# Optimization experiments

Measured on AMD Instinct MI355X. Metric: run time of the kernel, lower is better.

The kernel has to match this reference:

```python
import jax, jax.numpy as jnp
import numpy as np

HEADS = 8
DIM_HEAD = 64
SCALE = DIM_HEAD ** -0.5


def setup_inputs() -> dict:
    key = jax.random.key(0)
    k1, k2, k3 = jax.random.split(key, 3)
    b, p, n, dim = 2, 16, 512, 512
    inner = HEADS * DIM_HEAD  # 512
    x = jax.random.normal(k1, (b, p, n, dim), dtype=jnp.float32)
    W_qkv = jax.random.normal(k2, (dim, 3 * inner), dtype=jnp.float32) * (dim ** -0.5)
    W_out = jax.random.normal(k3, (inner, dim), dtype=jnp.float32) * (inner ** -0.5)
    b_out = jnp.zeros((dim,), dtype=jnp.float32)
    return {"x": x, "W_qkv": W_qkv, "W_out": W_out, "b_out": b_out}


def reference(x, W_qkv, W_out, b_out):
    b, p, n, dim = x.shape
    # QKV projection (no bias), split into q, k, v
    qkv = jnp.einsum('bpnd,de->bpne', x, W_qkv)
    q, k, v = jnp.split(qkv, 3, axis=-1)
    # (b, p, n, h*d) -> (b, p, h, n, d)
    def to_heads(t):
        return t.reshape(b, p, n, HEADS, DIM_HEAD).transpose(0, 1, 3, 2, 4)
    q, k, v = to_heads(q), to_heads(k), to_heads(v)
    # attention scores: (b, p, h, n, n)
    dots = jnp.einsum('bphnd,bphmd->bphnm', q, k) * SCALE
    attn = jax.nn.softmax(dots, axis=-1)
    out = jnp.einsum('bphnm,bphmd->bphnd', attn, v)
    # (b, p, h, n, d) -> (b, p, n, h*d)
    out = out.transpose(0, 1, 3, 2, 4).reshape(b, p, n, HEADS * DIM_HEAD)
    # output projection (dropout rate = 0.0 -> identity)
    return jnp.einsum('bpne,ed->bpnd', out, W_out) + b_out
```

## Files before the change

### kernel.cpp

```cpp
#include <hip/hip_runtime.h>
#include <hip/hip_bf16.h>

typedef short bf16x8 __attribute__((ext_vector_type(8)));
typedef short bf16x4 __attribute__((ext_vector_type(4)));
typedef float f32x4  __attribute__((ext_vector_type(4)));

__device__ __forceinline__ unsigned short f2bf(float f) {
    union { float fv; unsigned int u; } v; v.fv = f;
    unsigned int r = v.u + 0x7FFFu + ((v.u >> 16) & 1u);
    return (unsigned short)(r >> 16);
}

__device__ __forceinline__ short f2bf_n(float f) {
    union { __hip_bfloat16 h; short s; } u;
    u.h = __float2bfloat16(f);
    return u.s;
}

__device__ __forceinline__ void gload16(const short* g, short* l) {
    __builtin_amdgcn_global_load_lds(
        (const __attribute__((address_space(1))) void*)g,
        (__attribute__((address_space(3))) void*)l, 16, 0, 0);
}

__global__ __launch_bounds__(256) void cvt_x(
    const float* __restrict__ x, short* __restrict__ xb)
{
    size_t i = ((size_t)blockIdx.x * 256 + threadIdx.x) * 8;
    f32x4 a = *(const f32x4*)(x + i);
    f32x4 b = *(const f32x4*)(x + i + 4);
    bf16x8 s;
    #pragma unroll
    for (int e = 0; e < 4; ++e) { s[e] = (short)f2bf(a[e]); s[4 + e] = (short)f2bf(b[e]); }
    *(bf16x8*)(xb + i) = s;
}

__global__ __launch_bounds__(256) void tr_w2(
    const float* __restrict__ Wqkv, const float* __restrict__ Wout,
    short* __restrict__ Wqkvt, short* __restrict__ Woutt)
{
    __shared__ float tile[32][33];
    const int b = blockIdx.x;
    const float* src; short* dst; int N, bb;
    if (b < 768) { src = Wqkv; dst = Wqkvt; N = 1536; bb = b; }
    else         { src = Wout; dst = Woutt; N = 512;  bb = b - 768; }
    const int tx = threadIdx.x;
    const int nb = N >> 5;
    const int k0 = (bb / nb) * 32;
    const int n0 = (bb % nb) * 32;
    const int r  = tx >> 3;
    const int c4 = (tx & 7) * 4;
    f32x4 v = *(const f32x4*)(src + (size_t)(k0 + r) * N + n0 + c4);
    #pragma unroll
    for (int e = 0; e < 4; ++e) tile[r][c4 + e] = v[e];
    __syncthreads();
    bf16x4 o;
    #pragma unroll
    for (int e = 0; e < 4; ++e) o[e] = (short)f2bf(tile[c4 + e][r]);
    *(bf16x4*)(dst + (size_t)(n0 + r) * 512 + k0 + c4) = o;
}

template<int F32OUT>
__global__ __launch_bounds__(256, 2) void gemm_db(
    const short* __restrict__ A, const short* __restrict__ Bt,
    short* __restrict__ Cb, float* __restrict__ Cf, const float* __restrict__ bias,
    int M, int N, int K, int NB)
{
    __shared__ short lds[2][2][128 * 64];
    const int t    = threadIdx.x;
    const int lane = t & 63;
    const int wid  = t >> 6;
    const int l15  = lane & 15;
    const int lg   = lane >> 4;

    const int cpx = gridDim.x >> 3;
    const int swz = (blockIdx.x & 7) * cpx + (blockIdx.x >> 3);
    const int m0 = (swz / NB) * 128;
    const int n0 = (swz % NB) * 128;

    const int wm = (wid >> 1) * 64;
    const int wn = (wid & 1) * 64;

    const int scol = 8 * ((lane & 7) ^ ((lane >> 3) & 7));

    float bval[4];
    if constexpr (F32OUT) {
        #pragma unroll
        for (int ni = 0; ni < 4; ++ni) bval[ni] = bias[n0 + wn + ni * 16 + l15];
    }

    f32x4 acc[4][4];
    #pragma unroll
    for (int i = 0; i < 4; ++i)
        #pragma unroll
        for (int j = 0; j < 4; ++j)
            acc[i][j] = f32x4{0.f, 0.f, 0.f, 0.f};

    const int NT = K >> 6;

    auto stage = [&](int buf, int tk) {
        #pragma unroll
        for (int j = 0; j < 4; ++j) {
            const int r = wid * 32 + j * 8 + (lane >> 3);
            gload16(A  + (size_t)(m0 + r) * K + tk * 64 + scol,
                    &lds[buf][0][(wid * 32 + j * 8) * 64]);
            gload16(Bt + (size_t)(n0 + r) * K + tk * 64 + scol,
                    &lds[buf][1][(wid * 32 + j * 8) * 64]);
        }
    };

    stage(0, 0);

    for (int tk = 0; tk < NT; ++tk) {
        const int cur = tk & 1;
        if (tk + 1 < NT) {
            stage(cur ^ 1, tk + 1);
            asm volatile("s_waitcnt vmcnt(8)" ::: "memory");
        } else {
            asm volatile("s_waitcnt vmcnt(0)" ::: "memory");
        }
        __builtin_amdgcn_s_barrier();

        bf16x8 af[4][2], bg[4][2];
        #pragma unroll
        for (int kk = 0; kk < 2; ++kk) {
            #pragma unroll
            for (int mi = 0; mi < 4; ++mi)
                af[mi][kk] = *(const bf16x8*)&lds[cur][0][
                    (wm + mi * 16 + l15) * 64 + (((kk * 4 + lg) ^ (l15 & 7)) * 8)];
            #pragma unroll
            for (int ni = 0; ni < 4; ++ni)
                bg[ni][kk] = *(const bf16x8*)&lds[cur][1][
                    (wn + ni * 16 + l15) * 64 + (((kk * 4 + lg) ^ (l15 & 7)) * 8)];
        }

        __builtin_amdgcn_s_setprio(1);
        #pragma unroll
        for (int kk = 0; kk < 2; ++kk)
            #pragma unroll
            for (int mi = 0; mi < 4; ++mi)
                #pragma unroll
                for (int ni = 0; ni < 4; ++ni)
                    acc[mi][ni] = __builtin_amdgcn_mfma_f32_16x16x32_bf16(
                        af[mi][kk], bg[ni][kk], acc[mi][ni], 0, 0, 0);
        __builtin_amdgcn_s_setprio(0);
        __builtin_amdgcn_s_barrier();
    }

    #pragma unroll
    for (int mi = 0; mi < 4; ++mi) {
        #pragma unroll
        for (int ni = 0; ni < 4; ++ni) {
            const int col = n0 + wn + ni * 16 + l15;
            #pragma unroll
            for (int r = 0; r < 4; ++r) {
                const int rowi = m0 + wm + mi * 16 + 4 * lg + r;
                if constexpr (F32OUT) {
                    Cf[(size_t)rowi * N + col] = acc[mi][ni][r] + bval[ni];
                } else {
                    Cb[(size_t)rowi * N + col] = (short)f2bf(acc[mi][ni][r]);
                }
            }
        }
    }
}

__global__ __launch_bounds__(512, 4) void attn_kernel(
    const short* __restrict__ qkv, short* __restrict__ attn_out)
{
    __shared__ short Kl[2][4096];
    __shared__ short Vt[2][5120];
    const int t    = threadIdx.x;
    const int lane = t & 63;
    const int wid  = t >> 6;
    const int l15  = lane & 15;
    const int lg   = lane >> 4;
    const int pairid = blockIdx.x & 255;
    const int qh  = blockIdx.x >> 8;
    const int bp  = pairid >> 3;
    const int h   = pairid & 7;
    const size_t tok0 = (size_t)bp * 512;
    const int q0   = qh * 256 + wid * 32;
    const int qcol = h * 64;

    bf16x8 qf[2][2];
    #pragma unroll
    for (int mj = 0; mj < 2; ++mj)
        #pragma unroll
        for (int kf = 0; kf < 2; ++kf)
            qf[mj][kf] = *(const bf16x8*)(qkv + (tok0 + q0 + mj * 16 + l15) * 1536
                                          + qcol + kf * 32 + 8 * lg);

    f32x4 ot[4][2];
    #pragma unroll
    for (int i = 0; i < 4; ++i)
        #pragma unroll
        for (int j = 0; j < 2; ++j)
            ot[i][j] = f32x4{0.f, 0.f, 0.f, 0.f};
    float mrun[2] = {-1e30f, -1e30f}, lrun[2] = {0.f, 0.f};

    const int krow = t >> 3;
    const short* Ksrc0 = qkv + (tok0 + krow) * 1536 + 512 + qcol
                         + 8 * ((t & 7) ^ (krow & 7));
    const int sn = t >> 3;
    const int sd = (t & 7) * 8;
    const short* Vsrc0 = qkv + (tok0 + sn) * 1536 + 1024 + qcol + sd;
    const int kvp = (sn & 7) | (((sn >> 3) ^ (t & 7)) << 3);

    gload16(Ksrc0, &Kl[0][t * 8]);
    bf16x8 vreg = *(const bf16x8*)(Vsrc0);

    const float C = 0.18033688011112042f;

    for (int tkv = 0; tkv < 8; ++tkv) {
        const int cur = tkv & 1;
        #pragma unroll
        for (int i = 0; i < 8; ++i)
            Vt[cur][(sd + i) * 80 + kvp] = vreg[i];
        __syncthreads();
        if (tkv < 7) {
            gload16(Ksrc0 + (size_t)(tkv + 1) * 64 * 1536, &Kl[cur ^ 1][t * 8]);
            vreg = *(const bf16x8*)(Vsrc0 + (size_t)(tkv + 1) * 64 * 1536);
        }

        f32x4 st[4][2];
        #pragma unroll
        for (int i = 0; i < 4; ++i)
            #pragma unroll
            for (int j = 0; j < 2; ++j)
                st[i][j] = f32x4{0.f, 0.f, 0.f, 0.f};
        __builtin_amdgcn_s_setprio(1);
        #pragma unroll
        for (int kf = 0; kf < 2; ++kf) {
            #pragma unroll
            for (int ni = 0; ni < 4; ++ni) {
                bf16x8 kfr = *(const bf16x8*)&Kl[cur][
                    (ni * 16 + l15) * 64 + (((kf * 4 + lg) ^ (l15 & 7)) * 8)];
                #pragma unroll
                for (int mj = 0; mj < 2; ++mj)
                    st[ni][mj] = __builtin_amdgcn_mfma_f32_16x16x32_bf16(
                        kfr, qf[mj][kf], st[ni][mj], 0, 0, 0);
            }
        }
        __builtin_amdgcn_s_setprio(0);

        #pragma unroll
        for (int mj = 0; mj < 2; ++mj) {
            float pm = -1e30f;
            #pragma unroll
            for (int ni = 0; ni < 4; ++ni)
                #pragma unroll
                for (int r = 0; r < 4; ++r)
                    pm = fmaxf(pm, st[ni][mj][r]);
            pm = fmaxf(pm, __shfl_xor(pm, 16));
            pm = fmaxf(pm, __shfl_xor(pm, 32));
            pm *= C;
            if (!__all(pm <= mrun[mj] + 8.f)) {
                const float mnew = fmaxf(mrun[mj], pm);
                const float fsc  = __builtin_amdgcn_exp2f(mrun[mj] - mnew);
                lrun[mj] *= fsc;
                #pragma unroll
                for (int di = 0; di < 4; ++di) ot[di][mj] *= fsc;
                mrun[mj] = mnew;
            }
            float ps = 0.f;
            #pragma unroll
            for (int ni = 0; ni < 4; ++ni)
                #pragma unroll
                for (int r = 0; r < 4; ++r) {
                    float e = __builtin_amdgcn_exp2f(
                        __builtin_fmaf(st[ni][mj][r], C, -mrun[mj]));
                    st[ni][mj][r] = e;
                    ps += e;
                }
            ps += __shfl_xor(ps, 16);
            ps += __shfl_xor(ps, 32);
            lrun[mj] += ps;
        }

        __builtin_amdgcn_s_setprio(1);
        #pragma unroll
        for (int ni = 0; ni < 4; ++ni) {
            bf16x4 pb[2];
            #pragma unroll
            for (int mj = 0; mj < 2; ++mj)
                #pragma unroll
                for (int r = 0; r < 4; ++r)
                    pb[mj][r] = f2bf_n(st[ni][mj][r]);
            #pragma unroll
            for (int di = 0; di < 4; ++di) {
                const int row = di * 16 + l15;
                bf16x4 av = *(const bf16x4*)&Vt[cur][
                    row * 80
                    + (((2 * ni + (lg >> 1)) ^ (2 * di + (l15 >> 3))) * 8)
                    + 4 * (lg & 1)];
                #pragma unroll
                for (int mj = 0; mj < 2; ++mj)
                    ot[di][mj] = __builtin_amdgcn_mfma_f32_16x16x16bf16_1k(
                        av, pb[mj], ot[di][mj], 0, 0, 0);
            }
        }
        __builtin_amdgcn_s_setprio(0);
    }

    float inv[2];
    #pragma unroll
    for (int mj = 0; mj < 2; ++mj) inv[mj] = 1.f / lrun[mj];
    #pragma unroll
    for (int di = 0; di < 4; ++di)
        #pragma unroll
        for (int mj = 0; mj < 2; ++mj) {
            const size_t tok = tok0 + q0 + mj * 16 + l15;
            const int col = qcol + di * 16 + 4 * lg;
            bf16x4 o4;
            #pragma unroll
            for (int r = 0; r < 4; ++r)
                o4[r] = f2bf_n(ot[di][mj][r] * inv[mj]);
            *(bf16x4*)(attn_out + tok * 512 + col) = o4;
        }
}

extern "C" void kernel_launch(void* const* d_in, const int* in_sizes, int n_in,
                              void* d_out, int out_size, void* d_ws, size_t ws_size,
                              hipStream_t stream) {
    const float* x    = (const float*)d_in[0];
    const float* Wqkv = (const float*)d_in[1];
    const float* Wout = (const float*)d_in[2];
    const float* bout = (const float*)d_in[3];
    float* out = (float*)d_out;

    char* ws = (char*)d_ws;
    short* qkvb  = (short*)(ws);
    short* xb    = (short*)(ws + 50331648ull);
    short* attnb = xb;
    short* Wqkvt = (short*)(ws + 67108864ull);
    short* Woutt = (short*)(ws + 68681728ull);

    cvt_x<<<4096, 256, 0, stream>>>(x, xb);
    tr_w2<<<1024, 256, 0, stream>>>(Wqkv, Wout, Wqkvt, Woutt);

    gemm_db<0><<<1536, 256, 0, stream>>>(xb, Wqkvt, qkvb, nullptr, nullptr,
                                         16384, 1536, 512, 12);

    attn_kernel<<<512, 512, 0, stream>>>(qkvb, attnb);

    gemm_db<1><<<512, 256, 0, stream>>>(attnb, Woutt, nullptr, out, bout,
                                        16384, 512, 512, 4);
}
```

Measured before the change: 97.98 us.

## Software-pipeline QK^T of next tile with softmax and PV of previous tile

Restructures the attention KV loop so each iteration computes the QK^T scores for tile T, then runs softmax and the PV product for tile T-1. Score accumulators are double-buffered in registers and V is triple-buffered in shared memory, so the V tile used by PV is not overwritten by the next store. The goal is to overlap exp/softmax VALU work with MFMA work across tiles. In exchange it adds register pressure from a second score array and more LDS, which could lower occupancy at 4 blocks per CU.

Result: slower. 153.6 us (+56.7%).

```diff
diff --git a/kernel.cpp b/kernel.cpp
--- a/kernel.cpp
+++ b/kernel.cpp
@@ -169,7 +169,7 @@
     const short* __restrict__ qkv, short* __restrict__ attn_out)
 {
     __shared__ short Kl[2][4096];
-    __shared__ short Vt[2][5120];
+    __shared__ short Vt[3][5120];
     const int t    = threadIdx.x;
     const int lane = t & 63;
     const int wid  = t >> 6;
@@ -212,96 +212,108 @@
 
     const float C = 0.18033688011112042f;
 
-    for (int tkv = 0; tkv < 8; ++tkv) {
-        const int cur = tkv & 1;
-        #pragma unroll
-        for (int i = 0; i < 8; ++i)
-            Vt[cur][(sd + i) * 80 + kvp] = vreg[i];
-        __syncthreads();
-        if (tkv < 7) {
-            gload16(Ksrc0 + (size_t)(tkv + 1) * 64 * 1536, &Kl[cur ^ 1][t * 8]);
-            vreg = *(const bf16x8*)(Vsrc0 + (size_t)(tkv + 1) * 64 * 1536);
-        }
-
-        f32x4 st[4][2];
-        #pragma unroll
-        for (int i = 0; i < 4; ++i)
-            #pragma unroll
-            for (int j = 0; j < 2; ++j)
-                st[i][j] = f32x4{0.f, 0.f, 0.f, 0.f};
-        __builtin_amdgcn_s_setprio(1);
-        #pragma unroll
-        for (int kf = 0; kf < 2; ++kf) {
-            #pragma unroll
-            for (int ni = 0; ni < 4; ++ni) {
-                bf16x8 kfr = *(const bf16x8*)&Kl[cur][
-                    (ni * 16 + l15) * 64 + (((kf * 4 + lg) ^ (l15 & 7)) * 8)];
-                #pragma unroll
-                for (int mj = 0; mj < 2; ++mj)
-                    st[ni][mj] = __builtin_amdgcn_mfma_f32_16x16x32_bf16(
-                        kfr, qf[mj][kf], st[ni][mj], 0, 0, 0);
-            }
-        }
-        __builtin_amdgcn_s_setprio(0);
-
-        #pragma unroll
-        for (int mj = 0; mj < 2; ++mj) {
-            float pm = -1e30f;
-            #pragma unroll
-            for (int ni = 0; ni < 4; ++ni)
-                #pragma unroll
-                for (int r = 0; r < 4; ++r)
-                    pm = fmaxf(pm, st[ni][mj][r]);
-            pm = fmaxf(pm, __shfl_xor(pm, 16));
-            pm = fmaxf(pm, __shfl_xor(pm, 32));
-            pm *= C;
-            if (!__all(pm <= mrun[mj] + 8.f)) {
-                const float mnew = fmaxf(mrun[mj], pm);
-                const float fsc  = __builtin_amdgcn_exp2f(mrun[mj] - mnew);
-                lrun[mj] *= fsc;
-                #pragma unroll
-                for (int di = 0; di < 4; ++di) ot[di][mj] *= fsc;
-                mrun[mj] = mnew;
-            }
-            float ps = 0.f;
-            #pragma unroll
-            for (int ni = 0; ni < 4; ++ni)
-                #pragma unroll
-                for (int r = 0; r < 4; ++r) {
-                    float e = __builtin_amdgcn_exp2f(
-                        __builtin_fmaf(st[ni][mj][r], C, -mrun[mj]));
-                    st[ni][mj][r] = e;
-                    ps += e;
-                }
-            ps += __shfl_xor(ps, 16);
-            ps += __shfl_xor(ps, 32);
-            lrun[mj] += ps;
-        }
-
-        __builtin_amdgcn_s_setprio(1);
-        #pragma unroll
-        for (int ni = 0; ni < 4; ++ni) {
-            bf16x4 pb[2];
-            #pragma unroll
-            for (int mj = 0; mj < 2; ++mj)
-                #pragma unroll
-                for (int r = 0; r < 4; ++r)
-                    pb[mj][r] = f2bf_n(st[ni][mj][r]);
-            #pragma unroll
-            for (int di = 0; di < 4; ++di) {
-                const int row = di * 16 + l15;
-                bf16x4 av = *(const bf16x4*)&Vt[cur][
-                    row * 80
-                    + (((2 * ni + (lg >> 1)) ^ (2 * di + (l15 >> 3))) * 8)
-                    + 4 * (lg & 1)];
-                #pragma unroll
-                for (int mj = 0; mj < 2; ++mj)
-                    ot[di][mj] = __builtin_amdgcn_mfma_f32_16x16x16bf16_1k(
-                        av, pb[mj], ot[di][mj], 0, 0, 0);
-            }
-        }
-        __builtin_amdgcn_s_setprio(0);
-    }
+    f32x4 stA[4][2], stB[4][2];
+
+#define SMPV(ST, TP)                                                          \
+    {                                                                         \
+        const short* vsrc = &Vt[(TP) % 3][0];                                 \
+        _Pragma("unroll")                                                     \
+        for (int mj = 0; mj < 2; ++mj) {                                      \
+            float pm = -1e30f;                                                \
+            _Pragma("unroll")                                                 \
+            for (int ni = 0; ni < 4; ++ni)                                    \
+                _Pragma("unroll")                                             \
+                for (int r = 0; r < 4; ++r)                                   \
+                    pm = fmaxf(pm, ST[ni][mj][r]);                            \
+            pm = fmaxf(pm, __shfl_xor(pm, 16));                               \
+            pm = fmaxf(pm, __shfl_xor(pm, 32));                               \
+            pm *= C;                                                          \
+            if (!__all(pm <= mrun[mj] + 8.f)) {                               \
+                const float mnew = fmaxf(mrun[mj], pm);                       \
+                const float fsc  = __builtin_amdgcn_exp2f(mrun[mj] - mnew);   \
+                lrun[mj] *= fsc;                                              \
+                _Pragma("unroll")                                             \
+                for (int di = 0; di < 4; ++di) ot[di][mj] *= fsc;             \
+                mrun[mj] = mnew;                                              \
+            }                                                                 \
+            float ps = 0.f;                                                   \
+            _Pragma("unroll")                                                 \
+            for (int ni = 0; ni < 4; ++ni)                                    \
+                _Pragma("unroll")                                             \
+                for (int r = 0; r < 4; ++r) {                                 \
+                    float e = __builtin_amdgcn_exp2f(                         \
+                        __builtin_fmaf(ST[ni][mj][r], C, -mrun[mj]));         \
+                    ST[ni][mj][r] = e;                                        \
+                    ps += e;                                                  \
+                }                                                             \
+            ps += __shfl_xor(ps, 16);                                         \
+            ps += __shfl_xor(ps, 32);                                         \
+            lrun[mj] += ps;                                                   \
+        }                                                                     \
+        __builtin_amdgcn_s_setprio(1);                                        \
+        _Pragma("unroll")                                                     \
+        for (int ni = 0; ni < 4; ++ni) {                                      \
+            bf16x4 pb[2];                                                     \
+            _Pragma("unroll")                                                 \
+            for (int mj = 0; mj < 2; ++mj)                                    \
+                _Pragma("unroll")                                             \
+                for (int r = 0; r < 4; ++r)                                   \
+                    pb[mj][r] = f2bf_n(ST[ni][mj][r]);                        \
+            _Pragma("unroll")                                                 \
+            for (int di = 0; di < 4; ++di) {                                  \
+                bf16x4 av = *(const bf16x4*)&vsrc[                            \
+                    (di * 16 + l15) * 80                                      \
+                    + (((2 * ni + (lg >> 1)) ^ (2 * di + (l15 >> 3))) * 8)    \
+                    + 4 * (lg & 1)];                                          \
+                _Pragma("unroll")                                             \
+                for (int mj = 0; mj < 2; ++mj)                                \
+                    ot[di][mj] = __builtin_amdgcn_mfma_f32_16x16x16bf16_1k(   \
+                        av, pb[mj], ot[di][mj], 0, 0, 0);                     \
+            }                                                                 \
+        }                                                                     \
+        __builtin_amdgcn_s_setprio(0);                                        \
+    }
+
+#define BODY(T, SCUR, SPRV)                                                   \
+    {                                                                         \
+        short* vdst = &Vt[(T) % 3][0];                                        \
+        _Pragma("unroll")                                                     \
+        for (int i = 0; i < 8; ++i) vdst[(sd + i) * 80 + kvp] = vreg[i];      \
+        __syncthreads();                                                      \
+        if ((T) < 7) {                                                        \
+            gload16(Ksrc0 + (size_t)((T) + 1) * 64 * 1536,                    \
+                    &Kl[((T) + 1) & 1][t * 8]);                               \
+            vreg = *(const bf16x8*)(Vsrc0 + (size_t)((T) + 1) * 64 * 1536);   \
+        }                                                                     \
+        _Pragma("unroll")                                                     \
+        for (int i = 0; i < 4; ++i)                                           \
+            _Pragma("unroll")                                                 \
+            for (int j = 0; j < 2; ++j)                                       \
+                SCUR[i][j] = f32x4{0.f, 0.f, 0.f, 0.f};                       \
+        __builtin_amdgcn_s_setprio(1);                                        \
+        _Pragma("unroll")                                                     \
+        for (int kf = 0; kf < 2; ++kf) {                                      \
+            _Pragma("unroll")                                                 \
+            for (int ni = 0; ni < 4; ++ni) {                                  \
+                bf16x8 kfr = *(const bf16x8*)&Kl[(T) & 1][                    \
+                    (ni * 16 + l15) * 64 + (((kf * 4 + lg) ^ (l15 & 7)) * 8)];\
+                _Pragma("unroll")                                             \
+                for (int mj = 0; mj < 2; ++mj)                                \
+                    SCUR[ni][mj] = __builtin_amdgcn_mfma_f32_16x16x32_bf16(   \
+                        kfr, qf[mj][kf], SCUR[ni][mj], 0, 0, 0);              \
+            }                                                                 \
+        }                                                                     \
+        __builtin_amdgcn_s_setprio(0);                                        \
+        if ((T) > 0) SMPV(SPRV, (T) - 1);                                     \
+    }
+
+    for (int t2 = 0; t2 < 8; t2 += 2) {
+        BODY(t2, stA, stB);
+        BODY(t2 + 1, stB, stA);
+    }
+    SMPV(stB, 7);
+#undef BODY
+#undef SMPV
 
     float inv[2];
     #pragma unroll
```
